# Kernel tuning notes

Measured on AMD Instinct MI355X. Metric: run time of the kernel, lower is better.

## Reference

```python
import jax, jax.numpy as jnp
import numpy as np

D_MODEL = 1024
N_HEADS = 16
HEAD_DIM = D_MODEL // N_HEADS
SEQ_LEN = 2048
LN_EPS = 1e-5


def setup_inputs() -> dict:
    key = jax.random.key(0)
    ks = jax.random.split(key, 7)
    s = 1.0 / np.sqrt(D_MODEL)
    h = jax.random.normal(ks[0], (SEQ_LEN, D_MODEL), dtype=jnp.float32)
    # torch nn.Linear weights are (out_features, in_features)
    W_qkv = jax.random.uniform(ks[1], (3 * D_MODEL, D_MODEL), jnp.float32, -s, s)
    b_qkv = jax.random.uniform(ks[2], (3 * D_MODEL,), jnp.float32, -s, s)
    W_out = jax.random.uniform(ks[3], (D_MODEL, D_MODEL), jnp.float32, -s, s)
    b_out = jax.random.uniform(ks[4], (D_MODEL,), jnp.float32, -s, s)
    gamma = jnp.ones((D_MODEL,), jnp.float32)
    beta = jnp.zeros((D_MODEL,), jnp.float32)
    return {"h": h, "W_qkv": W_qkv, "b_qkv": b_qkv, "W_out": W_out,
            "b_out": b_out, "gamma": gamma, "beta": beta}


def reference(h, W_qkv, b_qkv, W_out, b_out, gamma, beta):
    S = h.shape[0]
    # QKV projection: (S, 3*D)
    qkv = h @ W_qkv.T + b_qkv
    q, k, v = jnp.split(qkv, 3, axis=-1)
    # (S, D) -> (H, S, Dh)
    q = q.reshape(S, N_HEADS, HEAD_DIM).transpose(1, 0, 2)
    k = k.reshape(S, N_HEADS, HEAD_DIM).transpose(1, 0, 2)
    v = v.reshape(S, N_HEADS, HEAD_DIM).transpose(1, 0, 2)
    # scaled dot-product attention, non-causal (matches F.sdpa defaults)
    scale = 1.0 / jnp.sqrt(jnp.asarray(HEAD_DIM, dtype=h.dtype))
    scores = jnp.einsum('hqd,hkd->hqk', q, k) * scale  # (H, S, S)
    attn = jax.nn.softmax(scores, axis=-1)
    attn_out = jnp.einsum('hqk,hkd->hqd', attn, v)     # (H, S, Dh)
    attn_out = attn_out.transpose(1, 0, 2).reshape(S, D_MODEL)
    # output projection + residual + LayerNorm
    attn_out = attn_out @ W_out.T + b_out
    x = h + attn_out
    mu = jnp.mean(x, axis=-1, keepdims=True)
    var = jnp.var(x, axis=-1, keepdims=True)
    x_norm = (x - mu) * jax.lax.rsqrt(var + LN_EPS)
    return x_norm * gamma + beta
```

## Files before the change

### kernel.cpp

```cpp
#include <hip/hip_runtime.h>
#include <stdint.h>

#define SEQ 2048
#define DM 1024
#define NH 16
#define DH 64
#define LN_EPS 1e-5f

typedef __bf16 bf16x8 __attribute__((ext_vector_type(8)));
typedef float f32x4 __attribute__((ext_vector_type(4)));
typedef unsigned short u16;
typedef unsigned short u16x8 __attribute__((ext_vector_type(8)));
typedef unsigned int u32;

__device__ __forceinline__ u16 f2bf(float f) {
  unsigned int u = __float_as_uint(f);
  unsigned int r = (u + 0x7fffu + ((u >> 16) & 1u)) >> 16;
  return (u16)r;
}

__device__ __forceinline__ float bf2f(u16 x) {
  return __uint_as_float(((u32)x) << 16);
}

__device__ __forceinline__ u32 packbf(float a, float b) {
  union { __bf16 h[2]; u32 u; } pw;
  pw.h[0] = (__bf16)a; pw.h[1] = (__bf16)b;
  return pw.u;
}

#define GLD_LDS16(gp, lp) __builtin_amdgcn_global_load_lds( \
  (const __attribute__((address_space(1))) void*)(gp),      \
  (__attribute__((address_space(3))) void*)(lp), 16, 0, 0)

__global__ __launch_bounds__(256) void k_f2bf(const float* __restrict__ in,
                                              u16* __restrict__ out, int n4) {
  int i = blockIdx.x * 256 + threadIdx.x;
  if (i >= n4) return;
  float4 v = reinterpret_cast<const float4*>(in)[i];
  ushort4 o;
  o.x = f2bf(v.x); o.y = f2bf(v.y); o.z = f2bf(v.z); o.w = f2bf(v.w);
  reinterpret_cast<ushort4*>(out)[i] = o;
}

template <int EPI, int BM, int BN>
__global__ __launch_bounds__(256)
void k_gemm_bt(const u16* __restrict__ A, const u16* __restrict__ B,
               const float* __restrict__ bias,
               u16* __restrict__ outb, u16* __restrict__ outv,
               float* __restrict__ outf, int M, int N, int K) {
  constexpr int MF = BM / 32, NF = BN / 32;
  constexpr int WM = BM / 2, WN = BN / 2;
  constexpr int AG = BM / 64, BG = BN / 64;
  __shared__ u16 Alds[2][BM][32];
  __shared__ u16 Blds[2][BN][32];
  const int tid = threadIdx.x;
  const int w = tid >> 6, l = tid & 63, lg = l >> 4, lr = l & 15;
  const int wr = w >> 1, wc = w & 1;
  const int m0 = blockIdx.y * BM, n0 = blockIdx.x * BN;
  const int KTall = K >> 5;
  const int ktn = KTall / gridDim.z;
  const int kt0 = blockIdx.z * ktn;

  f32x4 acc[MF][NF] = {};

  auto stage = [&](int buf, int kt) {
    const int k0 = kt << 5;
    const int row = l >> 2, col = (l & 3) * 8;
#pragma unroll
    for (int p = 0; p < AG; ++p) {
      const int rbase = (w * AG + p) * 16;
      GLD_LDS16(A + (size_t)(m0 + rbase + row) * K + k0 + col, &Alds[buf][rbase][0]);
    }
#pragma unroll
    for (int p = 0; p < BG; ++p) {
      const int rbase = (w * BG + p) * 16;
      GLD_LDS16(B + (size_t)(n0 + rbase + row) * K + k0 + col, &Blds[buf][rbase][0]);
    }
  };

  auto compute = [&](int buf) {
    bf16x8 af[MF], bfr[NF];
#pragma unroll
    for (int mi = 0; mi < MF; ++mi)
      af[mi] = *reinterpret_cast<const bf16x8*>(&Alds[buf][wr * WM + mi * 16 + lr][lg * 8]);
#pragma unroll
    for (int ni = 0; ni < NF; ++ni)
      bfr[ni] = *reinterpret_cast<const bf16x8*>(&Blds[buf][wc * WN + ni * 16 + lr][lg * 8]);
#pragma unroll
    for (int mi = 0; mi < MF; ++mi)
#pragma unroll
      for (int ni = 0; ni < NF; ++ni)
        acc[mi][ni] = __builtin_amdgcn_mfma_f32_16x16x32_bf16(af[mi], bfr[ni], acc[mi][ni], 0, 0, 0);
  };

  stage(0, kt0);
  __syncthreads();
  for (int i = 0; i < ktn; ++i) {
    const int cur = i & 1;
    if (i + 1 < ktn) stage(cur ^ 1, kt0 + i + 1);
    compute(cur);
    __syncthreads();
  }

  if (EPI == 3) {
    float* op = outf + (size_t)blockIdx.z * M * N;
#pragma unroll
    for (int ni = 0; ni < NF; ++ni) {
      const int n = n0 + wc * WN + ni * 16 + lr;
#pragma unroll
      for (int mi = 0; mi < MF; ++mi) {
#pragma unroll
        for (int r = 0; r < 4; ++r) {
          const int m = m0 + wr * WM + mi * 16 + lg * 4 + r;
          op[(size_t)m * N + n] = acc[mi][ni][r];
        }
      }
    }
  } else {
    if (n0 < 2048) {
#pragma unroll
      for (int ni = 0; ni < NF; ++ni) {
        const int n = n0 + wc * WN + ni * 16 + lr;
        const float bn = bias[n];
#pragma unroll
        for (int mi = 0; mi < MF; ++mi) {
#pragma unroll
          for (int r = 0; r < 4; ++r) {
            const int m = m0 + wr * WM + mi * 16 + lg * 4 + r;
            outb[(size_t)m * 2048 + n] = f2bf(acc[mi][ni][r] + bn);
          }
        }
      }
    } else {
#pragma unroll
      for (int ni = 0; ni < NF; ++ni) {
        const int n = n0 + wc * WN + ni * 16 + lr;
        const float bn = bias[n];
#pragma unroll
        for (int mi = 0; mi < MF; ++mi) {
          const int mb = m0 + wr * WM + mi * 16 + lg * 4;
          ushort4 pk;
          pk.x = f2bf(acc[mi][ni][0] + bn);
          pk.y = f2bf(acc[mi][ni][1] + bn);
          pk.z = f2bf(acc[mi][ni][2] + bn);
          pk.w = f2bf(acc[mi][ni][3] + bn);
          *reinterpret_cast<ushort4*>(&outv[(size_t)(n - 2048) * M + mb]) = pk;
        }
      }
    }
  }
}

template <int KSPLIT>
__global__ __launch_bounds__(256)
void k_attn(const u16* __restrict__ qk, const u16* __restrict__ vt,
            u16* __restrict__ Opart, float* __restrict__ lsum_out) {
  __shared__ u16 Klds[2][64 * 64];
  __shared__ u16 Vlds[2][64 * 64];
  __shared__ u16 Plds[4][16 * 64];
  const int tid = threadIdx.x;
  const int w = tid >> 6, l = tid & 63, lg = l >> 4, lr = l & 15;
  const int qb = blockIdx.x, h = blockIdx.y, sp = blockIdx.z;
  constexpr int NT = (SEQ / 64) / KSPLIT;
  const int kb0 = sp * NT;

  bf16x8 qf[2];
  {
    const size_t qrow = (size_t)(qb * 64 + w * 16 + lr) * 2048 + h * 64;
    qf[0] = *reinterpret_cast<const bf16x8*>(&qk[qrow + lg * 8]);
    qf[1] = *reinterpret_cast<const bf16x8*>(&qk[qrow + 32 + lg * 8]);
  }

  const int sr0 = w * 16 + (l >> 3);
  const int sc0 = ((l & 7) ^ (sr0 & 7)) * 8;
  const int sr1 = sr0 + 8;
  const int sc1 = ((l & 7) ^ (sr1 & 7)) * 8;
  const u16* kb_base = qk + 1024 + h * 64;
  const u16* vb_base = vt + (size_t)(h * 64) * 2048;

  auto stage = [&](int buf, int kb) {
    const u16* k0 = kb_base + (size_t)(kb * 64 + sr0) * 2048 + sc0;
    const u16* k1 = kb_base + (size_t)(kb * 64 + sr1) * 2048 + sc1;
    const u16* v0 = vb_base + (size_t)sr0 * 2048 + kb * 64 + sc0;
    const u16* v1 = vb_base + (size_t)sr1 * 2048 + kb * 64 + sc1;
    GLD_LDS16(k0, &Klds[buf][(w * 16) * 64]);
    GLD_LDS16(k1, &Klds[buf][(w * 16 + 8) * 64]);
    GLD_LDS16(v0, &Vlds[buf][(w * 16) * 64]);
    GLD_LDS16(v1, &Vlds[buf][(w * 16 + 8) * 64]);
  };

  auto kread = [&](int buf, int row, int kbyte) -> bf16x8 {
    const int off = row * 128 + (kbyte ^ ((row & 7) << 4));
    return *reinterpret_cast<const bf16x8*>(
        reinterpret_cast<const char*>(&Klds[buf][0]) + off);
  };
  auto vread = [&](int buf, int row, int kbyte) -> bf16x8 {
    const int off = row * 128 + (kbyte ^ ((row & 7) << 4));
    return *reinterpret_cast<const bf16x8*>(
        reinterpret_cast<const char*>(&Vlds[buf][0]) + off);
  };

  f32x4 oacc[4] = {};
  float lsum = 0.f;
  const float SC = 0.18033688011112042f;

  stage(0, kb0);
  __syncthreads();

  for (int t = 0; t < NT; ++t) {
    const int cur = t & 1;
    if (t + 1 < NT) stage(cur ^ 1, kb0 + t + 1);

    float p[4][4];
    __builtin_amdgcn_s_setprio(1);
#pragma unroll
    for (int nt = 0; nt < 4; ++nt) {
      bf16x8 kf0 = kread(cur, nt * 16 + lr, lg * 16);
      bf16x8 kf1 = kread(cur, nt * 16 + lr, 64 + lg * 16);
      f32x4 a = {};
      a = __builtin_amdgcn_mfma_f32_16x16x32_bf16(kf0, qf[0], a, 0, 0, 0);
      a = __builtin_amdgcn_mfma_f32_16x16x32_bf16(kf1, qf[1], a, 0, 0, 0);
#pragma unroll
      for (int r = 0; r < 4; ++r) {
        const float pv = exp2f(fmaf(a[r], SC, -8.0f));
        lsum += pv;
        p[nt][r] = pv;
      }
    }
    __builtin_amdgcn_s_setprio(0);

#pragma unroll
    for (int nt = 0; nt < 4; ++nt) {
      uint2 wv;
      wv.x = packbf(p[nt][0], p[nt][1]);
      wv.y = packbf(p[nt][2], p[nt][3]);
      const int pbyte = lr * 128 + ((nt * 32 + lg * 8) ^ ((lr & 7) << 4));
      *reinterpret_cast<uint2*>(reinterpret_cast<char*>(&Plds[w][0]) + pbyte) = wv;
    }

    __builtin_amdgcn_s_setprio(1);
#pragma unroll
    for (int kk = 0; kk < 2; ++kk) {
      const int abyte = lr * 128 + ((kk * 64 + lg * 16) ^ ((lr & 7) << 4));
      bf16x8 pa = *reinterpret_cast<const bf16x8*>(
          reinterpret_cast<const char*>(&Plds[w][0]) + abyte);
#pragma unroll
      for (int nd = 0; nd < 4; ++nd) {
        bf16x8 vf = vread(cur, nd * 16 + lr, kk * 64 + lg * 16);
        oacc[nd] = __builtin_amdgcn_mfma_f32_16x16x32_bf16(pa, vf, oacc[nd], 0, 0, 0);
      }
    }
    __builtin_amdgcn_s_setprio(0);
    __syncthreads();
  }

  float lt = lsum;
  lt += __shfl_xor(lt, 16);
  lt += __shfl_xor(lt, 32);
#pragma unroll
  for (int r = 0; r < 4; ++r) {
    const size_t orow = (size_t)sp * SEQ * DM +
                        (size_t)(qb * 64 + w * 16 + lg * 4 + r) * DM + h * 64;
#pragma unroll
    for (int nd = 0; nd < 4; ++nd)
      Opart[orow + nd * 16 + lr] = f2bf(oacc[nd][r]);
  }
  if (lg == 0)
    lsum_out[((size_t)sp * NH + h) * SEQ + qb * 64 + w * 16 + lr] = lt;
}

template <int KSPLIT>
__global__ __launch_bounds__(256)
void k_combine(const u16* __restrict__ Opart, const float* __restrict__ lsum,
               u16* __restrict__ attn_out) {
  const int row = blockIdx.x, tid = threadIdx.x;
  const int h = tid >> 4;
  float den = 0.f;
#pragma unroll
  for (int s = 0; s < KSPLIT; ++s)
    den += lsum[((size_t)s * NH + h) * SEQ + row];
  const float inv = 1.f / den;
  float o[4] = {0.f, 0.f, 0.f, 0.f};
#pragma unroll
  for (int s = 0; s < KSPLIT; ++s) {
    const ushort4 v = reinterpret_cast<const ushort4*>(
        Opart + ((size_t)s * SEQ + row) * DM)[tid];
    o[0] += bf2f(v.x); o[1] += bf2f(v.y);
    o[2] += bf2f(v.z); o[3] += bf2f(v.w);
  }
  ushort4 pk;
  pk.x = f2bf(o[0] * inv); pk.y = f2bf(o[1] * inv);
  pk.z = f2bf(o[2] * inv); pk.w = f2bf(o[3] * inv);
  reinterpret_cast<ushort4*>(attn_out + (size_t)row * DM)[tid] = pk;
}

__global__ __launch_bounds__(256)
void k_ln(const float* __restrict__ hin, const float* __restrict__ pp,
          const float* __restrict__ bout, const float* __restrict__ gamma,
          const float* __restrict__ beta, float* __restrict__ out) {
  const int row = blockIdx.x, tid = threadIdx.x;
  const float4 hv = reinterpret_cast<const float4*>(hin + (size_t)row * DM)[tid];
  const float4 p0 = reinterpret_cast<const float4*>(pp + (size_t)row * DM)[tid];
  const float4 p1 = reinterpret_cast<const float4*>(pp + (size_t)(SEQ + row) * DM)[tid];
  const float4 bv = reinterpret_cast<const float4*>(bout)[tid];
  float4 v;
  v.x = hv.x + p0.x + p1.x + bv.x;
  v.y = hv.y + p0.y + p1.y + bv.y;
  v.z = hv.z + p0.z + p1.z + bv.z;
  v.w = hv.w + p0.w + p1.w + bv.w;
  float s = v.x + v.y + v.z + v.w;
  float q = v.x * v.x + v.y * v.y + v.z * v.z + v.w * v.w;
#pragma unroll
  for (int m = 1; m < 64; m <<= 1) { s += __shfl_xor(s, m); q += __shfl_xor(q, m); }
  __shared__ float sh[8];
  const int w = tid >> 6;
  if ((tid & 63) == 0) { sh[w] = s; sh[4 + w] = q; }
  __syncthreads();
  s = sh[0] + sh[1] + sh[2] + sh[3];
  q = sh[4] + sh[5] + sh[6] + sh[7];
  const float mu = s * (1.f / 1024.f);
  const float var = q * (1.f / 1024.f) - mu * mu;
  const float rstd = rsqrtf(var + LN_EPS);
  float4 g = reinterpret_cast<const float4*>(gamma)[tid];
  float4 b = reinterpret_cast<const float4*>(beta)[tid];
  float4 o;
  o.x = (v.x - mu) * rstd * g.x + b.x;
  o.y = (v.y - mu) * rstd * g.y + b.y;
  o.z = (v.z - mu) * rstd * g.z + b.z;
  o.w = (v.w - mu) * rstd * g.w + b.w;
  reinterpret_cast<float4*>(out + (size_t)row * DM)[tid] = o;
}

extern "C" void kernel_launch(void* const* d_in, const int* in_sizes, int n_in,
                              void* d_out, int out_size, void* d_ws, size_t ws_size,
                              hipStream_t stream) {
  const float* h     = (const float*)d_in[0];
  const float* Wqkv  = (const float*)d_in[1];
  const float* bqkv  = (const float*)d_in[2];
  const float* Wout  = (const float*)d_in[3];
  const float* bout  = (const float*)d_in[4];
  const float* gamma = (const float*)d_in[5];
  const float* beta  = (const float*)d_in[6];
  float* out = (float*)d_out;

  char* ws = (char*)d_ws;
  u16* h_bf      = (u16*)(ws);
  u16* Wqkv_bf   = (u16*)(ws + (size_t)4 * 1024 * 1024);
  u16* Wout_bf   = (u16*)(ws + (size_t)10 * 1024 * 1024);
  u16* qk_bf     = (u16*)(ws + (size_t)12 * 1024 * 1024);
  u16* vt_bf     = (u16*)(ws + (size_t)20 * 1024 * 1024);
  u16* attn_bf   = (u16*)(ws + (size_t)24 * 1024 * 1024);
  u16* Opart     = (u16*)(ws + (size_t)28 * 1024 * 1024);
  float* Opp     = (float*)(ws + (size_t)36 * 1024 * 1024);
  float* lsums   = (float*)(ws + (size_t)52 * 1024 * 1024);

  k_f2bf<<<2048, 256, 0, stream>>>(h, h_bf, SEQ * DM / 4);
  k_f2bf<<<3072, 256, 0, stream>>>(Wqkv, Wqkv_bf, 3 * DM * DM / 4);
  k_f2bf<<<1024, 256, 0, stream>>>(Wout, Wout_bf, DM * DM / 4);

  k_gemm_bt<2, 64, 128><<<dim3(24, 32), 256, 0, stream>>>(
      h_bf, Wqkv_bf, bqkv, qk_bf, vt_bf, nullptr, SEQ, 3 * DM, DM);

  k_attn<2><<<dim3(SEQ / 64, NH, 2), 256, 0, stream>>>(qk_bf, vt_bf, Opart, lsums);
  k_combine<2><<<SEQ, 256, 0, stream>>>(Opart, lsums, attn_bf);

  k_gemm_bt<3, 64, 64><<<dim3(16, 32, 2), 256, 0, stream>>>(
      attn_bf, Wout_bf, nullptr, nullptr, nullptr, Opp, SEQ, DM, DM);

  k_ln<<<SEQ, 256, 0, stream>>>(h, Opp, bout, gamma, beta, out);
}
```

Before: 101.8 us.

## Fuse fp32-to-bf16 casts, remap blocks per XCD, store split-K partials as bf16

Merges the three conversion kernels into one launch and remaps block indices in both GEMMs and the attention kernel so each of the 8 XCDs gets a contiguous group of N-tiles or heads, aiming for better L2 reuse. The output-projection split-K partials are now written as bf16 instead of fp32, which halves that write and the LayerNorm read. In exchange, rounding the partials adds precision loss before the residual and LayerNorm.

After: 93.94 us. 7.7% less time.

```diff
diff --git a/kernel.cpp b/kernel.cpp
--- a/kernel.cpp
+++ b/kernel.cpp
@@ -33,22 +33,29 @@
   (const __attribute__((address_space(1))) void*)(gp),      \
   (__attribute__((address_space(3))) void*)(lp), 16, 0, 0)
 
-__global__ __launch_bounds__(256) void k_f2bf(const float* __restrict__ in,
-                                              u16* __restrict__ out, int n4) {
+__global__ __launch_bounds__(256)
+void k_f2bf3(const float* __restrict__ a, u16* __restrict__ oa, int na,
+             const float* __restrict__ b, u16* __restrict__ ob, int nb,
+             const float* __restrict__ c, u16* __restrict__ oc, int nc) {
   int i = blockIdx.x * 256 + threadIdx.x;
-  if (i >= n4) return;
-  float4 v = reinterpret_cast<const float4*>(in)[i];
+  const float* src;
+  u16* dst;
+  if (i < na) { src = a; dst = oa; }
+  else if (i < na + nb) { src = b; dst = ob; i -= na; }
+  else if (i < na + nb + nc) { src = c; dst = oc; i -= na + nb; }
+  else return;
+  float4 v = reinterpret_cast<const float4*>(src)[i];
   ushort4 o;
   o.x = f2bf(v.x); o.y = f2bf(v.y); o.z = f2bf(v.z); o.w = f2bf(v.w);
-  reinterpret_cast<ushort4*>(out)[i] = o;
-}
-
-template <int EPI, int BM, int BN>
+  reinterpret_cast<ushort4*>(dst)[i] = o;
+}
+
+template <int EPI, int BM, int BN, int XCDW>
 __global__ __launch_bounds__(256)
 void k_gemm_bt(const u16* __restrict__ A, const u16* __restrict__ B,
                const float* __restrict__ bias,
                u16* __restrict__ outb, u16* __restrict__ outv,
-               float* __restrict__ outf, int M, int N, int K) {
+               int M, int N, int K) {
   constexpr int MF = BM / 32, NF = BN / 32;
   constexpr int WM = BM / 2, WN = BN / 2;
   constexpr int AG = BM / 64, BG = BN / 64;
@@ -57,10 +64,22 @@
   const int tid = threadIdx.x;
   const int w = tid >> 6, l = tid & 63, lg = l >> 4, lr = l & 15;
   const int wr = w >> 1, wc = w & 1;
-  const int m0 = blockIdx.y * BM, n0 = blockIdx.x * BN;
+
+  int bx = blockIdx.x, by = blockIdx.y, bz = blockIdx.z;
+  if (XCDW > 0) {
+    const int nx = gridDim.x, ny = gridDim.y;
+    const int u = bx + nx * (by + ny * bz);
+    const int xcd = u & 7, g = u >> 3;
+    bx = xcd * XCDW + (g % XCDW);
+    const int rem = g / XCDW;
+    by = rem % ny;
+    bz = rem / ny;
+  }
+
+  const int m0 = by * BM, n0 = bx * BN;
   const int KTall = K >> 5;
   const int ktn = KTall / gridDim.z;
-  const int kt0 = blockIdx.z * ktn;
+  const int kt0 = bz * ktn;
 
   f32x4 acc[MF][NF] = {};
 
@@ -104,7 +123,7 @@
   }
 
   if (EPI == 3) {
-    float* op = outf + (size_t)blockIdx.z * M * N;
+    u16* op = outb + (size_t)bz * M * N;
 #pragma unroll
     for (int ni = 0; ni < NF; ++ni) {
       const int n = n0 + wc * WN + ni * 16 + lr;
@@ -113,7 +132,7 @@
 #pragma unroll
         for (int r = 0; r < 4; ++r) {
           const int m = m0 + wr * WM + mi * 16 + lg * 4 + r;
-          op[(size_t)m * N + n] = acc[mi][ni][r];
+          op[(size_t)m * N + n] = f2bf(acc[mi][ni][r]);
         }
       }
     }
@@ -161,7 +180,14 @@
   __shared__ u16 Plds[4][16 * 64];
   const int tid = threadIdx.x;
   const int w = tid >> 6, l = tid & 63, lg = l >> 4, lr = l & 15;
-  const int qb = blockIdx.x, h = blockIdx.y, sp = blockIdx.z;
+
+  const int u = blockIdx.x + 32 * (blockIdx.y + NH * blockIdx.z);
+  const int xcd = u & 7, g = u >> 3;
+  const int h = 2 * xcd + (g >> 6);
+  const int rem = g & 63;
+  const int sp = rem >> 5;
+  const int qb = rem & 31;
+
   constexpr int NT = (SEQ / 64) / KSPLIT;
   const int kb0 = sp * NT;
 
@@ -296,19 +322,19 @@
 }
 
 __global__ __launch_bounds__(256)
-void k_ln(const float* __restrict__ hin, const float* __restrict__ pp,
+void k_ln(const float* __restrict__ hin, const u16* __restrict__ pp,
           const float* __restrict__ bout, const float* __restrict__ gamma,
           const float* __restrict__ beta, float* __restrict__ out) {
   const int row = blockIdx.x, tid = threadIdx.x;
   const float4 hv = reinterpret_cast<const float4*>(hin + (size_t)row * DM)[tid];
-  const float4 p0 = reinterpret_cast<const float4*>(pp + (size_t)row * DM)[tid];
-  const float4 p1 = reinterpret_cast<const float4*>(pp + (size_t)(SEQ + row) * DM)[tid];
+  const ushort4 p0 = reinterpret_cast<const ushort4*>(pp + (size_t)row * DM)[tid];
+  const ushort4 p1 = reinterpret_cast<const ushort4*>(pp + (size_t)(SEQ + row) * DM)[tid];
   const float4 bv = reinterpret_cast<const float4*>(bout)[tid];
   float4 v;
-  v.x = hv.x + p0.x + p1.x + bv.x;
-  v.y = hv.y + p0.y + p1.y + bv.y;
-  v.z = hv.z + p0.z + p1.z + bv.z;
-  v.w = hv.w + p0.w + p1.w + bv.w;
+  v.x = hv.x + bf2f(p0.x) + bf2f(p1.x) + bv.x;
+  v.y = hv.y + bf2f(p0.y) + bf2f(p1.y) + bv.y;
+  v.z = hv.z + bf2f(p0.z) + bf2f(p1.z) + bv.z;
+  v.w = hv.w + bf2f(p0.w) + bf2f(p1.w) + bv.w;
   float s = v.x + v.y + v.z + v.w;
   float q = v.x * v.x + v.y * v.y + v.z * v.z + v.w * v.w;
 #pragma unroll
@@ -352,21 +378,21 @@
   u16* vt_bf     = (u16*)(ws + (size_t)20 * 1024 * 1024);
   u16* attn_bf   = (u16*)(ws + (size_t)24 * 1024 * 1024);
   u16* Opart     = (u16*)(ws + (size_t)28 * 1024 * 1024);
-  float* Opp     = (float*)(ws + (size_t)36 * 1024 * 1024);
-  float* lsums   = (float*)(ws + (size_t)52 * 1024 * 1024);
-
-  k_f2bf<<<2048, 256, 0, stream>>>(h, h_bf, SEQ * DM / 4);
-  k_f2bf<<<3072, 256, 0, stream>>>(Wqkv, Wqkv_bf, 3 * DM * DM / 4);
-  k_f2bf<<<1024, 256, 0, stream>>>(Wout, Wout_bf, DM * DM / 4);
-
-  k_gemm_bt<2, 64, 128><<<dim3(24, 32), 256, 0, stream>>>(
-      h_bf, Wqkv_bf, bqkv, qk_bf, vt_bf, nullptr, SEQ, 3 * DM, DM);
+  u16* Opp       = (u16*)(ws + (size_t)36 * 1024 * 1024);
+  float* lsums   = (float*)(ws + (size_t)44 * 1024 * 1024);
+
+  const int na = SEQ * DM / 4, nb = 3 * DM * DM / 4, nc = DM * DM / 4;
+  k_f2bf3<<<(na + nb + nc + 255) / 256, 256, 0, stream>>>(
+      h, h_bf, na, Wqkv, Wqkv_bf, nb, Wout, Wout_bf, nc);
+
+  k_gemm_bt<2, 64, 128, 3><<<dim3(24, 32), 256, 0, stream>>>(
+      h_bf, Wqkv_bf, bqkv, qk_bf, vt_bf, SEQ, 3 * DM, DM);
 
   k_attn<2><<<dim3(SEQ / 64, NH, 2), 256, 0, stream>>>(qk_bf, vt_bf, Opart, lsums);
   k_combine<2><<<SEQ, 256, 0, stream>>>(Opart, lsums, attn_bf);
 
-  k_gemm_bt<3, 64, 64><<<dim3(16, 32, 2), 256, 0, stream>>>(
-      attn_bf, Wout_bf, nullptr, nullptr, nullptr, Opp, SEQ, DM, DM);
+  k_gemm_bt<3, 64, 64, 2><<<dim3(16, 32, 2), 256, 0, stream>>>(
+      attn_bf, Wout_bf, nullptr, Opp, nullptr, SEQ, DM, DM);
 
   k_ln<<<SEQ, 256, 0, stream>>>(h, Opp, bout, gamma, beta, out);
 }
```
